# Performance work log

Hardware: AMD Instinct MI355X
Metric: run time of the kernel (lower is better)

The kernel has to match this reference:

```python
import jax, jax.numpy as jnp
import numpy as np
from jax import lax

H = 8          # num_heads
LAM = 4.0      # lambda_scale
POOL = 8       # pool_ratio (effective, N % POOL == 0)
NS_ITERS = 5
NS_EPS = 1e-4
WHITE_EPS = 1e-5


def _lap_kernel(x, y):
    # x: [B,H,n,D], y: [B,H,m,D] -> exp(-||x_i - y_j||_1 / LAM): [B,H,n,m]
    l1 = jnp.sum(jnp.abs(x[:, :, :, None, :] - y[:, :, None, :, :]), axis=-1)
    return jnp.exp(-l1 / LAM)


def setup_inputs() -> dict:
    key = jax.random.key(0)
    ks = jax.random.split(key, 8)
    B, N, C = 2, 1024, 512
    s = 0.05  # weight scale for realistic magnitudes
    return {
        "x": jax.random.normal(ks[0], (B, N, C), jnp.float32),
        "attention_mask": jnp.ones((B, N), jnp.float32),
        "qkv_w": jax.random.normal(ks[1], (3 * C, C), jnp.float32) * s,
        "qkv_b": jax.random.normal(ks[2], (3 * C,), jnp.float32) * s,
        "proj_w": jax.random.normal(ks[3], (C, C), jnp.float32) * s,
        "proj_b": jax.random.normal(ks[4], (C,), jnp.float32) * s,
        "dwc_w": jax.random.normal(ks[5], (C, 1, 3), jnp.float32) * s,
        "dwc_b": jax.random.normal(ks[6], (C,), jnp.float32) * s,
    }


def reference(x, attention_mask, qkv_w, qkv_b, proj_w, proj_b, dwc_w, dwc_b):
    B, N, C = x.shape
    D = C // H
    tm = attention_mask                      # [B,N]
    mh = tm[:, None, :, None]                # [B,1,N,1] broadcast over heads

    qkv = (x @ qkv_w.T + qkv_b).reshape(B, N, 3, H, D).transpose(2, 0, 3, 1, 4)
    q, k, v = qkv[0] * mh, qkv[1] * mh, qkv[2] * mh   # [B,H,N,D]

    # NOTE: faithful to source: raw reshape of [B,N,H*D] into [B,C,N]
    v_sp = v.transpose(0, 2, 1, 3).reshape(B, C, N)
    q_sp = q.transpose(0, 2, 1, 3).reshape(B, C, N)
    k_sp = k.transpose(0, 2, 1, 3).reshape(B, C, N)

    # depthwise conv1d, kernel 3, padding 1
    v_local = lax.conv_general_dilated(
        v_sp, dwc_w, window_strides=(1,), padding=[(1, 1)],
        feature_group_count=C, dimension_numbers=("NCH", "OIH", "NCH")
    ) + dwc_b[None, :, None]
    v_local = v_local.transpose(0, 2, 1) * tm[:, :, None]   # [B,N,C]

    p = POOL
    m = N // p
    pm = tm.reshape(B, 1, m, p).mean(-1)                    # [B,1,m]
    pms = jnp.clip(pm, 1e-6)
    q_pool = (q_sp * tm[:, None, :]).reshape(B, C, m, p).mean(-1) / pms
    k_pool = (k_sp * tm[:, None, :]).reshape(B, C, m, p).mean(-1) / pms
    lmask = (pm > 0).astype(x.dtype)[:, 0, :]               # [B,m]

    q_l = q_pool.transpose(0, 2, 1).reshape(B, m, H, D).transpose(0, 2, 1, 3)
    k_l = k_pool.transpose(0, 2, 1).reshape(B, m, H, D).transpose(0, 2, 1, 3)

    W = _lap_kernel(q_l, k_l)                               # [B,H,m,m]
    pair = lmask[:, None, :, None] * lmask[:, None, None, :]
    I = jnp.eye(m, dtype=x.dtype)[None, None]
    W = W * pair + I * (1.0 - pair)

    # Newton-Schulz pseudo-inverse
    W_eps = W + NS_EPS * I
    fro = jnp.sqrt(jnp.sum(W_eps * W_eps, axis=(-2, -1), keepdims=True))
    X = (2.0 / (fro + 1e-8)) * jnp.swapaxes(W_eps, -2, -1)
    for _ in range(NS_ITERS):
        X = X @ (2.0 * I - W_eps @ X)
    W_inv = X

    la_mask = lmask[:, None, None, :]                        # [B,1,1,m]
    C_q = _lap_kernel(q, k_l) * la_mask                      # [B,H,N,m]
    C_k = _lap_kernel(k, q_l) * la_mask                      # [B,H,N,m]

    # batch-statistics whitening of C_q over dims (0,2)
    qmask = tm[:, None, :, None]                             # [B,1,N,1]
    valid = jnp.clip(jnp.sum(qmask, axis=(0, 2), keepdims=True), 1.0)
    mu = jnp.sum(C_q * qmask, axis=(0, 2), keepdims=True) / valid
    cen = (C_q - mu) * qmask
    var = jnp.sum(cen * cen, axis=(0, 2), keepdims=True) / valid
    C_q_norm = ((C_q - mu) / jnp.sqrt(var + WHITE_EPS)) * qmask

    context = W_inv @ (jnp.swapaxes(C_k, -2, -1) @ v)        # [B,H,m,D]
    ga = (C_q_norm @ context) * mh                           # [B,H,N,D]
    ga = ga.transpose(0, 2, 1, 3).reshape(B, N, C)

    out = (ga + v_local) @ proj_w.T + proj_b
    return out * tm[:, :, None]
```

## Files before the change

### kernel.cpp

```cpp
#include <hip/hip_runtime.h>
#include <hip/hip_bf16.h>
#include <hip/hip_fp16.h>

#define Hh 8
#define Bz 2
#define Nn 1024
#define Cc 512
#define Dd 64
#define Mm 128
#define NS_EPS 1e-4f
#define WHITE_EPS 1e-5f
#define NEG_L2E_OVER_LAM (-0.3606737602222409f)

__device__ __forceinline__ float h2f(__half v) { return __half2float(v); }
__device__ __forceinline__ __half f2h(float v) { return __float2half(v); }
__device__ __forceinline__ float lapexp(float s) {
  return __builtin_amdgcn_exp2f(s * NEG_L2E_OVER_LAM);
}

typedef _Float16 half8 __attribute__((ext_vector_type(8)));
typedef _Float16 half4v __attribute__((ext_vector_type(4)));
typedef float float4v __attribute__((ext_vector_type(4)));

__global__ __launch_bounds__(256) void qkv_gemm(
    const float* __restrict__ x, const float* __restrict__ w,
    const float* __restrict__ bias, const float* __restrict__ tm,
    __half* __restrict__ Q, __half* __restrict__ K, __half* __restrict__ V) {
  __shared__ _Float16 As[128 * 40];
  __shared__ _Float16 Bs[128 * 40];
  int m0 = blockIdx.x * 128, n0 = blockIdx.y * 128;
  int tid = threadIdx.x;
  int lane = tid & 63, wv = tid >> 6;
  int wm = (wv >> 1) * 64, wn = (wv & 1) * 64;
  int l15 = lane & 15, quad = lane >> 4;
  int srow = tid >> 1, shalf = tid & 1;
  float4v acc[4][4] = {};
  for (int k0 = 0; k0 < 512; k0 += 32) {
    __syncthreads();
    {
      const float4* ga = (const float4*)(x + (size_t)(m0 + srow) * 512 + k0 + shalf * 16);
      const float4* gb = (const float4*)(w + (size_t)(n0 + srow) * 512 + k0 + shalf * 16);
      float4 a0 = ga[0], a1 = ga[1], a2 = ga[2], a3 = ga[3];
      float4 b0 = gb[0], b1 = gb[1], b2 = gb[2], b3 = gb[3];
      half8 ha0 = {(_Float16)a0.x, (_Float16)a0.y, (_Float16)a0.z, (_Float16)a0.w,
                   (_Float16)a1.x, (_Float16)a1.y, (_Float16)a1.z, (_Float16)a1.w};
      half8 ha1 = {(_Float16)a2.x, (_Float16)a2.y, (_Float16)a2.z, (_Float16)a2.w,
                   (_Float16)a3.x, (_Float16)a3.y, (_Float16)a3.z, (_Float16)a3.w};
      half8 hb0 = {(_Float16)b0.x, (_Float16)b0.y, (_Float16)b0.z, (_Float16)b0.w,
                   (_Float16)b1.x, (_Float16)b1.y, (_Float16)b1.z, (_Float16)b1.w};
      half8 hb1 = {(_Float16)b2.x, (_Float16)b2.y, (_Float16)b2.z, (_Float16)b2.w,
                   (_Float16)b3.x, (_Float16)b3.y, (_Float16)b3.z, (_Float16)b3.w};
      int lo = srow * 40 + shalf * 16;
      *(half8*)&As[lo] = ha0;
      *(half8*)&As[lo + 8] = ha1;
      *(half8*)&Bs[lo] = hb0;
      *(half8*)&Bs[lo + 8] = hb1;
    }
    __syncthreads();
    half8 a[4], b[4];
#pragma unroll
    for (int mt = 0; mt < 4; ++mt)
      a[mt] = *(const half8*)&As[(wm + mt * 16 + l15) * 40 + quad * 8];
#pragma unroll
    for (int nt = 0; nt < 4; ++nt)
      b[nt] = *(const half8*)&Bs[(wn + nt * 16 + l15) * 40 + quad * 8];
#pragma unroll
    for (int mt = 0; mt < 4; ++mt)
#pragma unroll
      for (int nt = 0; nt < 4; ++nt)
        acc[mt][nt] =
            __builtin_amdgcn_mfma_f32_16x16x32_f16(a[mt], b[nt], acc[mt][nt], 0, 0, 0);
  }
#pragma unroll
  for (int mt = 0; mt < 4; ++mt) {
#pragma unroll
    for (int r = 0; r < 4; ++r) {
      int row = m0 + wm + mt * 16 + quad * 4 + r;
      int b_ = row >> 10, n_ = row & 1023;
      float t = tm[b_ * 1024 + n_];
#pragma unroll
      for (int nt = 0; nt < 4; ++nt) {
        int c3 = n0 + wn + nt * 16 + l15;
        float v = (acc[mt][nt][r] + bias[c3]) * t;
        int sec = c3 >> 9, ch = c3 & 511;
        __half* dst = (sec == 0) ? Q : (sec == 1 ? K : V);
        dst[(size_t)b_ * (Nn * Cc) + (size_t)n_ * 512 + ch] = f2h(v);
      }
    }
  }
}

__global__ __launch_bounds__(256) void fused_phase1(
    const __half* __restrict__ Q, const __half* __restrict__ K,
    const __half* __restrict__ V, const float* __restrict__ tm,
    __half* __restrict__ Wh, float* __restrict__ KTVp,
    float* __restrict__ PS, __half* __restrict__ Pbuf) {
  __shared__ __align__(16) char smem[31232];
  int id = blockIdx.x;
  int tid = threadIdx.x;
  if (id < 512) {
    int jt = id & 3, bh = (id >> 2) & 15, nc = id >> 6;
    int b = bh >> 3, h = bh & 7;
    int j0 = jt * 32;
    float* kls = (float*)smem;
    float* Qs  = (float*)(smem + 8704);
    float* red = (float*)(smem + 17408);
    float* tms = (float*)(smem + 20480);
    float* pmi = (float*)(smem + 21504);
    float* lmv = (float*)(smem + 21632);
    int u0 = j0 * 8;
    tms[tid] = tm[b * 1024 + u0 + tid];
    __syncthreads();
    if (tid < 32) {
      float pm = 0.f;
#pragma unroll
      for (int i = 0; i < 8; ++i) pm += tms[tid * 8 + i];
      pm *= 0.125f;
      pmi[tid] = 0.125f / fmaxf(pm, 1e-6f);
      lmv[tid] = (pm > 0.f) ? 1.f : 0.f;
    }
    __syncthreads();
    {
      const __half* Kb = K + (size_t)b * (Nn * Cc) + (size_t)(h * 64) * 1024;
      int jl = tid >> 3, cq = tid & 7;
      float pv = pmi[jl];
      float r[8];
#pragma unroll
      for (int i = 0; i < 8; ++i) {
        int c = cq * 8 + i;
        half8 v = *(const half8*)(Kb + (size_t)c * 1024 + u0 + jl * 8);
        float s = 0.f;
#pragma unroll
        for (int xx = 0; xx < 8; ++xx) s += (float)v[xx] * tms[jl * 8 + xx];
        r[i] = s * pv;
      }
      float4 w0 = {r[0], r[1], r[2], r[3]};
      float4 w1 = {r[4], r[5], r[6], r[7]};
      *(float4*)&kls[jl * 68 + cq * 8] = w0;
      *(float4*)&kls[jl * 68 + cq * 8 + 4] = w1;
    }
    int sr = tid >> 3, sd8 = (tid & 7) * 8;
    int jq = tid & 15, nq = tid >> 4;
    float lmA = 0.f, lmB = 0.f;
    float aA1 = 0.f, aA2 = 0.f, aA3 = 0.f, aB1 = 0.f, aB2 = 0.f, aB3 = 0.f;
    int jA = j0 + jq * 2, jB = jA + 1;
    for (int nt = 0; nt < 4; ++nt) {
      int n0 = nc * 128 + nt * 32;
      __syncthreads();
      if (nt == 0) { lmA = lmv[jq * 2]; lmB = lmv[jq * 2 + 1]; }
      {
        size_t gi = (size_t)b * (Nn * Cc) + (size_t)(n0 + sr) * 512 + h * 64 + sd8;
        half8 kv = *(const half8*)(Q + gi);
        float4 k0 = {(float)kv[0], (float)kv[1], (float)kv[2], (float)kv[3]};
        float4 k1 = {(float)kv[4], (float)kv[5], (float)kv[6], (float)kv[7]};
        *(float4*)&Qs[sr * 68 + sd8] = k0;
        *(float4*)&Qs[sr * 68 + sd8 + 4] = k1;
      }
      __syncthreads();
      const float4* q0p = (const float4*)&kls[(jq * 2) * 68];
      const float4* q1p = (const float4*)&kls[(jq * 2 + 1) * 68];
      const float4* k0p = (const float4*)&Qs[(nq * 2) * 68];
      const float4* k1p = (const float4*)&Qs[(nq * 2 + 1) * 68];
      float s00 = 0.f, s01 = 0.f, s10 = 0.f, s11 = 0.f;
#pragma unroll
      for (int i = 0; i < 16; ++i) {
        int dq = (i + tid) & 15;
        float4 q0 = q0p[dq], q1 = q1p[dq];
        float4 k0 = k0p[dq], k1 = k1p[dq];
        s00 += fabsf(q0.x - k0.x) + fabsf(q0.y - k0.y) + fabsf(q0.z - k0.z) + fabsf(q0.w - k0.w);
        s01 += fabsf(q0.x - k1.x) + fabsf(q0.y - k1.y) + fabsf(q0.z - k1.z) + fabsf(q0.w - k1.w);
        s10 += fabsf(q1.x - k0.x) + fabsf(q1.y - k0.y) + fabsf(q1.z - k0.z) + fabsf(q1.w - k0.w);
        s11 += fabsf(q1.x - k1.x) + fabsf(q1.y - k1.y) + fabsf(q1.z - k1.z) + fabsf(q1.w - k1.w);
      }
      int nA = n0 + nq * 2, nB = nA + 1;
      float tA = tm[b * 1024 + nA], tB = tm[b * 1024 + nB];
      float xAa = lapexp(s00) * lmA;
      float xAb = lapexp(s01) * lmA;
      float xBa = lapexp(s10) * lmB;
      float xBb = lapexp(s11) * lmB;
      __half2 pA; pA.x = f2h(xAa); pA.y = f2h(xBa);
      __half2 pB; pB.x = f2h(xAb); pB.y = f2h(xBb);
      *(__half2*)&Pbuf[((size_t)bh * 1024 + nA) * 128 + jA] = pA;
      *(__half2*)&Pbuf[((size_t)bh * 1024 + nB) * 128 + jA] = pB;
      float xt;
      xt = xAa * tA; aA1 += xt; aA2 += xt * xt; aA3 += xt * tA;
      xt = xAb * tB; aA1 += xt; aA2 += xt * xt; aA3 += xt * tB;
      xt = xBa * tA; aB1 += xt; aB2 += xt * xt; aB3 += xt * tA;
      xt = xBb * tB; aB1 += xt; aB2 += xt * xt; aB3 += xt * tB;
    }
    int jl = jq * 2;
    red[(jl * 8 + nq) * 3 + 0] = aA1;
    red[(jl * 8 + nq) * 3 + 1] = aA2;
    red[(jl * 8 + nq) * 3 + 2] = aA3;
    red[((jl + 1) * 8 + nq) * 3 + 0] = aB1;
    red[((jl + 1) * 8 + nq) * 3 + 1] = aB2;
    red[((jl + 1) * 8 + nq) * 3 + 2] = aB3;
    __syncthreads();
    if (tid < 32) {
      float s1 = 0.f, s2 = 0.f, s3 = 0.f;
#pragma unroll
      for (int q = 0; q < 8; ++q) {
        s1 += red[(tid * 8 + q) * 3 + 0];
        s2 += red[(tid * 8 + q) * 3 + 1];
        s3 += red[(tid * 8 + q) * 3 + 2];
      }
      size_t base = ((size_t)(nc * 16 + bh) * 128 + j0 + tid) * 3;
      PS[base] = s1; PS[base + 1] = s2; PS[base + 2] = s3;
    }
  } else if (id < 1024) {
    int kid = id - 512;
    int jt = kid & 7, bh = (kid >> 3) & 15, nc = kid >> 7;
    int b = bh >> 3, h = bh & 7;
    int j0 = jt * 16;
    float* qls = (float*)smem;
    float* Ks  = (float*)(smem + 4352);
    float* Vs  = (float*)(smem + 13056);
    float* P   = (float*)(smem + 21760);
    float* tms = (float*)(smem + 24320);
    float* pmi = (float*)(smem + 24832);
    float* lmv = (float*)(smem + 24896);
    int u0 = j0 * 8;
    if (tid < 128) tms[tid] = tm[b * 1024 + u0 + tid];
    __syncthreads();
    if (tid < 16) {
      float pm = 0.f;
#pragma unroll
      for (int i = 0; i < 8; ++i) pm += tms[tid * 8 + i];
      pm *= 0.125f;
      pmi[tid] = 0.125f / fmaxf(pm, 1e-6f);
      lmv[tid] = (pm > 0.f) ? 1.f : 0.f;
    }
    __syncthreads();
    {
      const __half* Qb = Q + (size_t)b * (Nn * Cc) + (size_t)(h * 64) * 1024;
      int jl_ = tid >> 4, cq = tid & 15;
      float pv = pmi[jl_];
      float r[4];
#pragma unroll
      for (int i = 0; i < 4; ++i) {
        int c = cq * 4 + i;
        half8 v = *(const half8*)(Qb + (size_t)c * 1024 + u0 + jl_ * 8);
        float s = 0.f;
#pragma unroll
        for (int xx = 0; xx < 8; ++xx) s += (float)v[xx] * tms[jl_ * 8 + xx];
        r[i] = s * pv;
      }
      float4 w0 = {r[0], r[1], r[2], r[3]};
      *(float4*)&qls[jl_ * 68 + cq * 4] = w0;
    }
    int sr = tid >> 3, sd8 = (tid & 7) * 8;
    int jq = tid & 15, nq = tid >> 4;
    int jl = tid >> 4, dq4 = tid & 15;
    float acc[4] = {};
    for (int nt = 0; nt < 8; ++nt) {
      int n0 = nc * 256 + nt * 32;
      __syncthreads();
      {
        size_t gi = (size_t)b * (Nn * Cc) + (size_t)(n0 + sr) * 512 + h * 64 + sd8;
        half8 kv = *(const half8*)(K + gi);
        half8 vv = *(const half8*)(V + gi);
        float4 k0 = {(float)kv[0], (float)kv[1], (float)kv[2], (float)kv[3]};
        float4 k1 = {(float)kv[4], (float)kv[5], (float)kv[6], (float)kv[7]};
        float4 v0 = {(float)vv[0], (float)vv[1], (float)vv[2], (float)vv[3]};
        float4 v1 = {(float)vv[4], (float)vv[5], (float)vv[6], (float)vv[7]};
        *(float4*)&Ks[sr * 68 + sd8] = k0;
        *(float4*)&Ks[sr * 68 + sd8 + 4] = k1;
        *(float4*)&Vs[sr * 68 + sd8] = v0;
        *(float4*)&Vs[sr * 68 + sd8 + 4] = v1;
      }
      __syncthreads();
      {
        const float4* qp = (const float4*)&qls[jq * 68];
        const float4* k0p = (const float4*)&Ks[(nq * 2) * 68];
        const float4* k1p = (const float4*)&Ks[(nq * 2 + 1) * 68];
        float s0 = 0.f, s1 = 0.f;
#pragma unroll
        for (int i = 0; i < 16; ++i) {
          int dq = (i + tid) & 15;
          float4 qv = qp[dq];
          float4 k0 = k0p[dq], k1 = k1p[dq];
          s0 += fabsf(qv.x - k0.x) + fabsf(qv.y - k0.y) + fabsf(qv.z - k0.z) + fabsf(qv.w - k0.w);
          s1 += fabsf(qv.x - k1.x) + fabsf(qv.y - k1.y) + fabsf(qv.z - k1.z) + fabsf(qv.w - k1.w);
        }
        P[(nq * 2) * 20 + jq] = lapexp(s0);
        P[(nq * 2 + 1) * 20 + jq] = lapexp(s1);
      }
      __syncthreads();
      {
#pragma unroll 8
        for (int n = 0; n < 32; ++n) {
          float p = P[n * 20 + jl];
          float4 v = *(const float4*)&Vs[n * 68 + dq4 * 4];
          acc[0] += p * v.x; acc[1] += p * v.y; acc[2] += p * v.z; acc[3] += p * v.w;
        }
      }
    }
    {
      float lm = lmv[jl];
      float* dst = &KTVp[((size_t)nc * 16 + bh) * 8192 + (size_t)(j0 + jl) * 64 + dq4 * 4];
      float4 o = {acc[0] * lm, acc[1] * lm, acc[2] * lm, acc[3] * lm};
      *(float4*)dst = o;
    }
  } else {
    int wid = id - 1024;
    int it = wid >> 4, bh = wid & 15;
    int b = bh >> 3, h = bh & 7;
    int i0 = it * 16;
    _Float16* kls16 = (_Float16*)smem;
    float* qs  = (float*)(smem + 18432);
    float* pm2 = (float*)(smem + 22784);
    float* tms = (float*)(smem + 23808);
    _Float16* ps16 = (_Float16*)(smem + 23808);
    for (int e = tid; e < 1024; e += 256) tms[e] = tm[b * 1024 + e];
    __syncthreads();
    if (tid < 128) {
      float pm = 0.f;
#pragma unroll
      for (int i = 0; i < 8; ++i) pm += tms[tid * 8 + i];
      pm *= 0.125f;
      pm2[tid * 2] = 0.125f / fmaxf(pm, 1e-6f);
      pm2[tid * 2 + 1] = (pm > 0.f) ? 1.f : 0.f;
    }
    __syncthreads();
    {
      const __half* Kb = K + (size_t)b * (Nn * Cc) + (size_t)(h * 64) * 1024;
      const __half* Qb = Q + (size_t)b * (Nn * Cc) + (size_t)(h * 64) * 1024;
#pragma unroll
      for (int k = 0; k < 4; ++k) {
        int g = k * 256 + tid;
        int j = g >> 3, cq = g & 7;
        float pv = pm2[j * 2];
        _Float16 r[8];
#pragma unroll
        for (int i = 0; i < 8; ++i) {
          int c = cq * 8 + i;
          half8 v = *(const half8*)(Kb + (size_t)c * 1024 + j * 8);
          float s = 0.f;
#pragma unroll
          for (int xx = 0; xx < 8; ++xx) s += (float)v[xx] * tms[j * 8 + xx];
          r[i] = (_Float16)(s * pv);
        }
        half8 w0 = {r[0], r[1], r[2], r[3], r[4], r[5], r[6], r[7]};
        *(half8*)&kls16[j * 72 + cq * 8] = w0;
      }
      {
        int il = tid >> 4, cq = tid & 15;
        float pv = pm2[(i0 + il) * 2];
        float r[4];
#pragma unroll
        for (int i = 0; i < 4; ++i) {
          int c = cq * 4 + i;
          half8 v = *(const half8*)(Qb + (size_t)c * 1024 + (i0 + il) * 8);
          float s = 0.f;
#pragma unroll
          for (int xx = 0; xx < 8; ++xx) s += (float)v[xx] * tms[(i0 + il) * 8 + xx];
          r[i] = s * pv;
        }
        float4 w0 = {r[0], r[1], r[2], r[3]};
        *(float4*)&qs[il * 68 + cq * 4] = w0;
      }
    }
    __syncthreads();
    int jg = tid & 63, ng = tid >> 6;
    int j = jg * 2;
    const _Float16* kArow = &kls16[j * 72];
    const _Float16* kBrow = &kls16[(j + 1) * 72];
    float sA[4] = {}, sB[4] = {};
#pragma unroll
    for (int i = 0; i < 16; ++i) {
      int dq = (i + jg) & 15;
      half4v k4a = *(const half4v*)&kArow[dq * 4];
      half4v k4b = *(const half4v*)&kBrow[dq * 4];
      float4 ka = {(float)k4a[0], (float)k4a[1], (float)k4a[2], (float)k4a[3]};
      float4 kb = {(float)k4b[0], (float)k4b[1], (float)k4b[2], (float)k4b[3]};
#pragma unroll
      for (int r = 0; r < 4; ++r) {
        float4 qv = *(const float4*)&qs[(ng * 4 + r) * 68 + dq * 4];
        sA[r] += fabsf(qv.x - ka.x) + fabsf(qv.y - ka.y) + fabsf(qv.z - ka.z) + fabsf(qv.w - ka.w);
        sB[r] += fabsf(qv.x - kb.x) + fabsf(qv.y - kb.y) + fabsf(qv.z - kb.z) + fabsf(qv.w - kb.w);
      }
    }
    float lmA = pm2[j * 2 + 1], lmB = pm2[(j + 1) * 2 + 1];
#pragma unroll
    for (int r = 0; r < 4; ++r) {
      int i = i0 + ng * 4 + r;
      float lmi = pm2[i * 2 + 1];
      float prA = lmi * lmA, prB = lmi * lmB;
      float dA = (i == j) ? 1.f : 0.f;
      float dB = (i == j + 1) ? 1.f : 0.f;
      ps16[(ng * 4 + r) * 132 + j] =
          (_Float16)(lapexp(sA[r]) * prA + dA * (1.f - prA) + dA * NS_EPS);
      ps16[(ng * 4 + r) * 132 + j + 1] =
          (_Float16)(lapexp(sB[r]) * prB + dB * (1.f - prB) + dB * NS_EPS);
    }
    __syncthreads();
    for (int e = tid; e < 2048; e += 256) {
      _Float16 v = ps16[(e >> 7) * 132 + (e & 127)];
      Wh[(size_t)bh * (Mm * Mm) + (size_t)(i0 + (e >> 7)) * 128 + (e & 127)] =
          *(__half*)&v;
    }
  }
}

__global__ __launch_bounds__(1024) void fused_phase2(
    const __half* __restrict__ Wh, const float* __restrict__ KTVp,
    const float* __restrict__ PS, const float* __restrict__ tm,
    __half* __restrict__ CTX, float* __restrict__ MU, float* __restrict__ RS) {
  __shared__ __align__(16) char smem[143360];
  int tid = threadIdx.x;
  if (blockIdx.x < 16) {
    int bh = blockIdx.x;
    _Float16* Ws = (_Float16*)smem;
    _Float16* Xa = (_Float16*)(smem + 34816);
    _Float16* Xb = (_Float16*)(smem + 69632);
    _Float16* Tt = (_Float16*)(smem + 104448);
    float* red = (float*)(smem + 139264);
    const __half* Wb = Wh + (size_t)bh * 16384;
    float fro = 0.f;
    for (int e = tid; e < 16384; e += 1024) {
      float wv = h2f(Wb[e]);
      Ws[(e >> 7) * 136 + (e & 127)] = (_Float16)wv;
      fro += wv * wv;
    }
    red[tid] = fro;
    __syncthreads();
    for (int off = 512; off > 0; off >>= 1) {
      if (tid < off) red[tid] += red[tid + off];
      __syncthreads();
    }
    float scale = 2.f / (sqrtf(red[0]) + 1e-8f);
    for (int e = tid; e < 16384; e += 1024) {
      int i = e >> 7, k = e & 127;
      Xa[i * 136 + k] = (_Float16)(scale * (float)Ws[k * 136 + i]);
      Xb[i * 136 + k] = (_Float16)(scale * (float)Ws[i * 136 + k]);
    }
    __syncthreads();
    int lane = tid & 63, wv_ = tid >> 6;
    int wm = (wv_ >> 2) * 32, wn = (wv_ & 3) * 32;
    int l15 = lane & 15, quad = lane >> 4;
    for (int it = 0; it < 5; ++it) {
      {
        float4v acc[2][2] = {};
#pragma unroll
        for (int kt = 0; kt < 4; ++kt) {
          half8 a[2], b[2];
#pragma unroll
          for (int mt = 0; mt < 2; ++mt)
            a[mt] = *(const half8*)&Ws[(wm + mt * 16 + l15) * 136 + kt * 32 + quad * 8];
#pragma unroll
          for (int nt = 0; nt < 2; ++nt)
            b[nt] = *(const half8*)&Xb[(wn + nt * 16 + l15) * 136 + kt * 32 + quad * 8];
#pragma unroll
          for (int mt = 0; mt < 2; ++mt)
#pragma unroll
            for (int nt = 0; nt < 2; ++nt)
              acc[mt][nt] =
                  __builtin_amdgcn_mfma_f32_16x16x32_f16(a[mt], b[nt], acc[mt][nt], 0, 0, 0);
        }
#pragma unroll
        for (int mt = 0; mt < 2; ++mt)
#pragma unroll
          for (int r = 0; r < 4; ++r) {
            int i = wm + mt * 16 + quad * 4 + r;
#pragma unroll
            for (int nt = 0; nt < 2; ++nt) {
              int j = wn + nt * 16 + l15;
              Tt[j * 136 + i] = (_Float16)(((i == j) ? 2.f : 0.f) - acc[mt][nt][r]);
            }
          }
      }
      __syncthreads();
      {
        float4v acc[2][2] = {};
#pragma unroll
        for (int kt = 0; kt < 4; ++kt) {
          half8 a[2], b[2];
#pragma unroll
          for (int mt = 0; mt < 2; ++mt)
            a[mt] = *(const half8*)&Xa[(wm + mt * 16 + l15) * 136 + kt * 32 + quad * 8];
#pragma unroll
          for (int nt = 0; nt < 2; ++nt)
            b[nt] = *(const half8*)&Tt[(wn + nt * 16 + l15) * 136 + kt * 32 + quad * 8];
#pragma unroll
          for (int mt = 0; mt < 2; ++mt)
#pragma unroll
            for (int nt = 0; nt < 2; ++nt)
              acc[mt][nt] =
                  __builtin_amdgcn_mfma_f32_16x16x32_f16(a[mt], b[nt], acc[mt][nt], 0, 0, 0);
        }
        __syncthreads();
#pragma unroll
        for (int mt = 0; mt < 2; ++mt)
#pragma unroll
          for (int r = 0; r < 4; ++r) {
            int i = wm + mt * 16 + quad * 4 + r;
#pragma unroll
            for (int nt = 0; nt < 2; ++nt) {
              int j = wn + nt * 16 + l15;
              _Float16 v = (_Float16)acc[mt][nt][r];
              Xa[i * 136 + j] = v;
              Xb[j * 136 + i] = v;
            }
          }
      }
      __syncthreads();
    }
    float* KTVs = (float*)smem;
    for (int e = tid; e < 8192; e += 1024) {
      float s = KTVp[(size_t)bh * 8192 + e];
#pragma unroll
      for (int nc = 1; nc < 4; ++nc) s += KTVp[((size_t)nc * 16 + bh) * 8192 + e];
      KTVs[(e >> 6) * 68 + (e & 63)] = s;
    }
    __syncthreads();
    int i = tid >> 3, d0 = (tid & 7) * 8;
    float a0 = 0.f, a1 = 0.f, a2 = 0.f, a3 = 0.f;
    float a4 = 0.f, a5 = 0.f, a6 = 0.f, a7 = 0.f;
#pragma unroll 4
    for (int j = 0; j < 128; ++j) {
      float xv = (float)Xa[i * 136 + j];
      float4 k0 = *(const float4*)&KTVs[j * 68 + d0];
      float4 k1 = *(const float4*)&KTVs[j * 68 + d0 + 4];
      a0 += xv * k0.x; a1 += xv * k0.y; a2 += xv * k0.z; a3 += xv * k0.w;
      a4 += xv * k1.x; a5 += xv * k1.y; a6 += xv * k1.z; a7 += xv * k1.w;
    }
    half8 hout = {(_Float16)a0, (_Float16)a1, (_Float16)a2, (_Float16)a3,
                  (_Float16)a4, (_Float16)a5, (_Float16)a6, (_Float16)a7};
    *(half8*)(CTX + (size_t)bh * 8192 + (size_t)i * 64 + d0) = hout;
  } else {
    float (*red2)[2] = (float(*)[2])smem;
    float* ts = (float*)(smem + 8192);
    float a = 0.f, c = 0.f;
    for (int i = tid; i < 2048; i += 1024) { float t = tm[i]; a += t; c += t * t; }
    red2[tid][0] = a; red2[tid][1] = c;
    __syncthreads();
    for (int off = 512; off > 0; off >>= 1) {
      if (tid < off) { red2[tid][0] += red2[tid + off][0]; red2[tid][1] += red2[tid + off][1]; }
      __syncthreads();
    }
    if (tid == 0) { ts[0] = red2[0][0]; ts[1] = red2[0][1]; }
    __syncthreads();
    int hj = tid;
    int h = hj >> 7, j = hj & 127;
    float s1 = 0.f, s2 = 0.f, s3 = 0.f;
#pragma unroll
    for (int nc = 0; nc < 8; ++nc)
#pragma unroll
      for (int b = 0; b < 2; ++b) {
        const float* p = PS + ((size_t)(nc * 16 + b * 8 + h) * 128 + j) * 3;
        s1 += p[0]; s2 += p[1]; s3 += p[2];
      }
    float valid = fmaxf(ts[0], 1.f);
    float mu = s1 / valid;
    float var = (s2 - 2.f * mu * s3 + mu * mu * ts[1]) / valid;
    var = fmaxf(var, 0.f);
    MU[hj] = mu;
    RS[hj] = rsqrtf(var + WHITE_EPS);
  }
}

__global__ __launch_bounds__(256) void ga_fused(
    const __half* __restrict__ Pbuf, const float* __restrict__ MU,
    const float* __restrict__ RS, const __half* __restrict__ CTXg,
    const __half* __restrict__ V, const float* __restrict__ dwc_w,
    const float* __restrict__ dwc_b, const float* __restrict__ tm,
    __half* __restrict__ VL) {
  int bh = blockIdx.y;
  int b = bh >> 3, h = bh & 7;
  int n0 = blockIdx.x * 32;
  __shared__ __half Ps[32][130];
  __shared__ __align__(16) __half2 ctx2[128][32];
  __shared__ float musr[128][2];
  int tid = threadIdx.x;
  for (int e = tid; e < 4096; e += 256)
    Ps[e >> 7][e & 127] = Pbuf[((size_t)bh * 1024 + n0 + (e >> 7)) * 128 + (e & 127)];
  {
    const __half2* cg = (const __half2*)(CTXg + (size_t)bh * 8192);
    for (int e = tid; e < 4096; e += 256) ctx2[e >> 5][e & 31] = cg[e];
  }
  if (tid < 128) { musr[tid][0] = MU[h * 128 + tid]; musr[tid][1] = RS[h * 128 + tid]; }
  __syncthreads();
  int nn = tid >> 4, dq = tid & 15;
  float acc[2][4] = {};
#pragma unroll 2
  for (int j = 0; j < 128; ++j) {
    float mu = musr[j][0], rs = musr[j][1];
    uint2 cc = *(const uint2*)&ctx2[j][dq * 2];
    __half2 c01 = __builtin_bit_cast(__half2, cc.x);
    __half2 c23 = __builtin_bit_cast(__half2, cc.y);
    float c0 = h2f(c01.x), c1 = h2f(c01.y), c2 = h2f(c23.x), c3 = h2f(c23.y);
#pragma unroll
    for (int rr = 0; rr < 2; ++rr) {
      float pj = (h2f(Ps[nn + rr * 16][j]) - mu) * rs;
      acc[rr][0] += pj * c0; acc[rr][1] += pj * c1;
      acc[rr][2] += pj * c2; acc[rr][3] += pj * c3;
    }
  }
#pragma unroll
  for (int rr = 0; rr < 2; ++rr) {
    int t = n0 + nn + rr * 16;
    float tmv = tm[b * 1024 + t];
    float t2 = tmv * tmv;
    float o[4] = {acc[rr][0] * t2, acc[rr][1] * t2, acc[rr][2] * t2, acc[rr][3] * t2};
#pragma unroll
    for (int q = 0; q < 4; ++q) {
      int c = h * 64 + dq * 4 + q;
      float vacc = dwc_b[c];
#pragma unroll
      for (int k = 0; k < 3; ++k) {
        int u = t - 1 + k;
        if (u >= 0 && u < 1024) {
          int n = 2 * c + (u >> 9), ch = u & 511;
          vacc += dwc_w[c * 3 + k] * h2f(V[(size_t)b * (Nn * Cc) + (size_t)n * 512 + ch]);
        }
      }
      o[q] += vacc * tmv;
    }
    size_t base = (size_t)b * (Nn * Cc) + (size_t)t * 512 + h * 64 + dq * 4;
    VL[base] = f2h(o[0]);
    VL[base + 1] = f2h(o[1]);
    VL[base + 2] = f2h(o[2]);
    VL[base + 3] = f2h(o[3]);
  }
}

__global__ __launch_bounds__(256) void proj_gemm(
    const __half* __restrict__ Ain, const float* __restrict__ w,
    const float* __restrict__ bias, const float* __restrict__ tm,
    float* __restrict__ out) {
  __shared__ _Float16 As[64 * 40];
  __shared__ _Float16 Bs[64 * 40];
  int m0 = blockIdx.x * 64, n0 = blockIdx.y * 64;
  int tid = threadIdx.x;
  int lane = tid & 63, wv = tid >> 6;
  int wm = (wv >> 1) * 32, wn = (wv & 1) * 32;
  int l15 = lane & 15, quad = lane >> 4;
  int srow = tid >> 2, scol = (tid & 3) * 8;
  float4v acc[2][2] = {};
  for (int k0 = 0; k0 < 512; k0 += 32) {
    __syncthreads();
    {
      half8 ha = *(const half8*)(Ain + (size_t)(m0 + srow) * 512 + k0 + scol);
      const float4* gb = (const float4*)(w + (size_t)(n0 + srow) * 512 + k0 + scol);
      float4 b0 = gb[0], b1 = gb[1];
      half8 hb = {(_Float16)b0.x, (_Float16)b0.y, (_Float16)b0.z, (_Float16)b0.w,
                  (_Float16)b1.x, (_Float16)b1.y, (_Float16)b1.z, (_Float16)b1.w};
      int lo = srow * 40 + scol;
      *(half8*)&As[lo] = ha;
      *(half8*)&Bs[lo] = hb;
    }
    __syncthreads();
    half8 a[2], b[2];
#pragma unroll
    for (int mt = 0; mt < 2; ++mt)
      a[mt] = *(const half8*)&As[(wm + mt * 16 + l15) * 40 + quad * 8];
#pragma unroll
    for (int nt = 0; nt < 2; ++nt)
      b[nt] = *(const half8*)&Bs[(wn + nt * 16 + l15) * 40 + quad * 8];
#pragma unroll
    for (int mt = 0; mt < 2; ++mt)
#pragma unroll
      for (int nt = 0; nt < 2; ++nt)
        acc[mt][nt] =
            __builtin_amdgcn_mfma_f32_16x16x32_f16(a[mt], b[nt], acc[mt][nt], 0, 0, 0);
  }
#pragma unroll
  for (int mt = 0; mt < 2; ++mt) {
#pragma unroll
    for (int r = 0; r < 4; ++r) {
      int row = m0 + wm + mt * 16 + quad * 4 + r;
      int b_ = row >> 10, n_ = row & 1023;
      float t = tm[b_ * 1024 + n_];
#pragma unroll
      for (int nt = 0; nt < 2; ++nt) {
        int co = n0 + wn + nt * 16 + l15;
        out[(size_t)row * 512 + co] = (acc[mt][nt][r] + bias[co]) * t;
      }
    }
  }
}

extern "C" void kernel_launch(void* const* d_in, const int* in_sizes, int n_in,
                              void* d_out, int out_size, void* d_ws, size_t ws_size,
                              hipStream_t stream) {
  const float* x      = (const float*)d_in[0];
  const float* tm     = (const float*)d_in[1];
  const float* qkv_w  = (const float*)d_in[2];
  const float* qkv_b  = (const float*)d_in[3];
  const float* proj_w = (const float*)d_in[4];
  const float* proj_b = (const float*)d_in[5];
  const float* dwc_w  = (const float*)d_in[6];
  const float* dwc_b  = (const float*)d_in[7];
  float* out = (float*)d_out;

  char* wsb = (char*)d_ws;
  __half* Qh  = (__half*)(wsb + 0);
  __half* Kh  = (__half*)(wsb + 2097152);
  __half* Vh  = (__half*)(wsb + 4194304);
  __half* VLh = (__half*)(wsb + 6291456);
  float*  KTVp = (float*)(wsb + 6291456);
  float*  MU  = (float*)(wsb + 8913920);
  float*  RS  = (float*)(wsb + 8918016);
  __half* CTX = (__half*)(wsb + 8922112);
  float*  PS  = (float*)(wsb + 9184256);
  __half* Wh  = (__half*)(wsb + 9380864);

  __half* Pbuf = (__half*)d_out;

  qkv_gemm<<<dim3(16, 12), 256, 0, stream>>>(x, qkv_w, qkv_b, tm, Qh, Kh, Vh);
  fused_phase1<<<1152, 256, 0, stream>>>(Qh, Kh, Vh, tm, Wh, KTVp, PS, Pbuf);
  fused_phase2<<<17, 1024, 0, stream>>>(Wh, KTVp, PS, tm, CTX, MU, RS);
  ga_fused<<<dim3(32, 16), 256, 0, stream>>>(Pbuf, MU, RS, CTX, Vh, dwc_w, dwc_b, tm, VLh);
  proj_gemm<<<dim3(32, 8), 256, 0, stream>>>(VLh, proj_w, proj_b, tm, out);
}
```

Before: 197.5 us.

## Compute L1 distances in packed fp16 with dot2 and reorder block roles

Replaces the fp32 L1-distance inner loops in all three phase-1 block roles with packed fp16 subtraction, a sign-bit mask and fdot2 accumulation into fp32. Operands are now staged in LDS as fp16 instead of being widened to fp32, which cuts shared-memory footprint and traffic and the count of ALU instructions per distance. The W-matrix blocks, previously last in the grid, are moved to the front so the heavier per-block work starts early. The cost is extra rounding in the differences, since pooled q/k values are rounded to fp16 before subtraction, which could change accuracy in the exponent.

```diff
diff --git a/kernel.cpp b/kernel.cpp
--- a/kernel.cpp
+++ b/kernel.cpp
@@ -20,7 +20,22 @@
 
 typedef _Float16 half8 __attribute__((ext_vector_type(8)));
 typedef _Float16 half4v __attribute__((ext_vector_type(4)));
+typedef _Float16 half2v __attribute__((ext_vector_type(2)));
+typedef unsigned int uint4v __attribute__((ext_vector_type(4)));
 typedef float float4v __attribute__((ext_vector_type(4)));
+
+__device__ __forceinline__ float l1dot(half8 a, half8 b, float s) {
+  half8 d = a - b;
+  uint4v u = __builtin_bit_cast(uint4v, d);
+  u &= 0x7FFF7FFFu;
+  const half2v one = {(_Float16)1.f, (_Float16)1.f};
+#pragma unroll
+  for (int p = 0; p < 4; ++p) {
+    half2v dv = __builtin_bit_cast(half2v, (unsigned int)u[p]);
+    s = __builtin_amdgcn_fdot2(dv, one, s, false);
+  }
+  return s;
+}
 
 __global__ __launch_bounds__(256) void qkv_gemm(
     const float* __restrict__ x, const float* __restrict__ w,
@@ -95,19 +110,115 @@
     const __half* __restrict__ V, const float* __restrict__ tm,
     __half* __restrict__ Wh, float* __restrict__ KTVp,
     float* __restrict__ PS, __half* __restrict__ Pbuf) {
-  __shared__ __align__(16) char smem[31232];
+  __shared__ __align__(16) char smem[25984];
   int id = blockIdx.x;
   int tid = threadIdx.x;
-  if (id < 512) {
-    int jt = id & 3, bh = (id >> 2) & 15, nc = id >> 6;
+  if (id < 128) {
+    int it = id >> 4, bh = id & 15;
+    int b = bh >> 3, h = bh & 7;
+    int i0 = it * 16;
+    _Float16* kls16 = (_Float16*)smem;
+    _Float16* qs16 = (_Float16*)(smem + 18432);
+    float* pm2 = (float*)(smem + 20736);
+    float* tms = (float*)(smem + 21760);
+    _Float16* ps16 = (_Float16*)(smem + 21760);
+    for (int e = tid; e < 1024; e += 256) tms[e] = tm[b * 1024 + e];
+    __syncthreads();
+    if (tid < 128) {
+      float pm = 0.f;
+#pragma unroll
+      for (int i = 0; i < 8; ++i) pm += tms[tid * 8 + i];
+      pm *= 0.125f;
+      pm2[tid * 2] = 0.125f / fmaxf(pm, 1e-6f);
+      pm2[tid * 2 + 1] = (pm > 0.f) ? 1.f : 0.f;
+    }
+    __syncthreads();
+    {
+      const __half* Kb = K + (size_t)b * (Nn * Cc) + (size_t)(h * 64) * 1024;
+      const __half* Qb = Q + (size_t)b * (Nn * Cc) + (size_t)(h * 64) * 1024;
+#pragma unroll
+      for (int k = 0; k < 4; ++k) {
+        int g = k * 256 + tid;
+        int j = g >> 3, cq = g & 7;
+        float pv = pm2[j * 2];
+        _Float16 r[8];
+#pragma unroll
+        for (int i = 0; i < 8; ++i) {
+          int c = cq * 8 + i;
+          half8 v = *(const half8*)(Kb + (size_t)c * 1024 + j * 8);
+          float s = 0.f;
+#pragma unroll
+          for (int xx = 0; xx < 8; ++xx) s += (float)v[xx] * tms[j * 8 + xx];
+          r[i] = (_Float16)(s * pv);
+        }
+        half8 w0 = {r[0], r[1], r[2], r[3], r[4], r[5], r[6], r[7]};
+        *(half8*)&kls16[j * 72 + cq * 8] = w0;
+      }
+      {
+        int il = tid >> 4, cq = tid & 15;
+        float pv = pm2[(i0 + il) * 2];
+        _Float16 r[4];
+#pragma unroll
+        for (int i = 0; i < 4; ++i) {
+          int c = cq * 4 + i;
+          half8 v = *(const half8*)(Qb + (size_t)c * 1024 + (i0 + il) * 8);
+          float s = 0.f;
+#pragma unroll
+          for (int xx = 0; xx < 8; ++xx) s += (float)v[xx] * tms[(i0 + il) * 8 + xx];
+          r[i] = (_Float16)(s * pv);
+        }
+        half4v w0 = {r[0], r[1], r[2], r[3]};
+        *(half4v*)&qs16[il * 72 + cq * 4] = w0;
+      }
+    }
+    __syncthreads();
+    int jg = tid & 63, ng = tid >> 6;
+    int j = jg * 2;
+    const half8* kAp = (const half8*)&kls16[j * 72];
+    const half8* kBp = (const half8*)&kls16[(j + 1) * 72];
+    float sA[4] = {}, sB[4] = {};
+#pragma unroll
+    for (int i = 0; i < 8; ++i) {
+      int dq = (i + jg) & 7;
+      half8 ka = kAp[dq];
+      half8 kb = kBp[dq];
+#pragma unroll
+      for (int r = 0; r < 4; ++r) {
+        half8 qv = *(const half8*)&qs16[(ng * 4 + r) * 72 + dq * 8];
+        sA[r] = l1dot(qv, ka, sA[r]);
+        sB[r] = l1dot(qv, kb, sB[r]);
+      }
+    }
+    float lmA = pm2[j * 2 + 1], lmB = pm2[(j + 1) * 2 + 1];
+#pragma unroll
+    for (int r = 0; r < 4; ++r) {
+      int i = i0 + ng * 4 + r;
+      float lmi = pm2[i * 2 + 1];
+      float prA = lmi * lmA, prB = lmi * lmB;
+      float dA = (i == j) ? 1.f : 0.f;
+      float dB = (i == j + 1) ? 1.f : 0.f;
+      ps16[(ng * 4 + r) * 132 + j] =
+          (_Float16)(lapexp(sA[r]) * prA + dA * (1.f - prA) + dA * NS_EPS);
+      ps16[(ng * 4 + r) * 132 + j + 1] =
+          (_Float16)(lapexp(sB[r]) * prB + dB * (1.f - prB) + dB * NS_EPS);
+    }
+    __syncthreads();
+    for (int e = tid; e < 2048; e += 256) {
+      _Float16 v = ps16[(e >> 7) * 132 + (e & 127)];
+      Wh[(size_t)bh * (Mm * Mm) + (size_t)(i0 + (e >> 7)) * 128 + (e & 127)] =
+          *(__half*)&v;
+    }
+  } else if (id < 640) {
+    int sid = id - 128;
+    int jt = sid & 3, bh = (sid >> 2) & 15, nc = sid >> 6;
     int b = bh >> 3, h = bh & 7;
     int j0 = jt * 32;
-    float* kls = (float*)smem;
-    float* Qs  = (float*)(smem + 8704);
-    float* red = (float*)(smem + 17408);
-    float* tms = (float*)(smem + 20480);
-    float* pmi = (float*)(smem + 21504);
-    float* lmv = (float*)(smem + 21632);
+    _Float16* kls16 = (_Float16*)smem;
+    _Float16* Qs16 = (_Float16*)(smem + 4608);
+    float* red = (float*)(smem + 9216);
+    float* tms = (float*)(smem + 12288);
+    float* pmi = (float*)(smem + 13312);
+    float* lmv = (float*)(smem + 13440);
     int u0 = j0 * 8;
     tms[tid] = tm[b * 1024 + u0 + tid];
     __syncthreads();
@@ -124,7 +235,7 @@
       const __half* Kb = K + (size_t)b * (Nn * Cc) + (size_t)(h * 64) * 1024;
       int jl = tid >> 3, cq = tid & 7;
       float pv = pmi[jl];
-      float r[8];
+      _Float16 r[8];
 #pragma unroll
       for (int i = 0; i < 8; ++i) {
         int c = cq * 8 + i;
@@ -132,12 +243,10 @@
         float s = 0.f;
 #pragma unroll
         for (int xx = 0; xx < 8; ++xx) s += (float)v[xx] * tms[jl * 8 + xx];
-        r[i] = s * pv;
-      }
-      float4 w0 = {r[0], r[1], r[2], r[3]};
-      float4 w1 = {r[4], r[5], r[6], r[7]};
-      *(float4*)&kls[jl * 68 + cq * 8] = w0;
-      *(float4*)&kls[jl * 68 + cq * 8 + 4] = w1;
+        r[i] = (_Float16)(s * pv);
+      }
+      half8 w0 = {r[0], r[1], r[2], r[3], r[4], r[5], r[6], r[7]};
+      *(half8*)&kls16[jl * 72 + cq * 8] = w0;
     }
     int sr = tid >> 3, sd8 = (tid & 7) * 8;
     int jq = tid & 15, nq = tid >> 4;
@@ -151,26 +260,23 @@
       {
         size_t gi = (size_t)b * (Nn * Cc) + (size_t)(n0 + sr) * 512 + h * 64 + sd8;
         half8 kv = *(const half8*)(Q + gi);
-        float4 k0 = {(float)kv[0], (float)kv[1], (float)kv[2], (float)kv[3]};
-        float4 k1 = {(float)kv[4], (float)kv[5], (float)kv[6], (float)kv[7]};
-        *(float4*)&Qs[sr * 68 + sd8] = k0;
-        *(float4*)&Qs[sr * 68 + sd8 + 4] = k1;
-      }
-      __syncthreads();
-      const float4* q0p = (const float4*)&kls[(jq * 2) * 68];
-      const float4* q1p = (const float4*)&kls[(jq * 2 + 1) * 68];
-      const float4* k0p = (const float4*)&Qs[(nq * 2) * 68];
-      const float4* k1p = (const float4*)&Qs[(nq * 2 + 1) * 68];
+        *(half8*)&Qs16[sr * 72 + sd8] = kv;
+      }
+      __syncthreads();
+      const half8* q0p = (const half8*)&kls16[(jq * 2) * 72];
+      const half8* q1p = (const half8*)&kls16[(jq * 2 + 1) * 72];
+      const half8* k0p = (const half8*)&Qs16[(nq * 2) * 72];
+      const half8* k1p = (const half8*)&Qs16[(nq * 2 + 1) * 72];
       float s00 = 0.f, s01 = 0.f, s10 = 0.f, s11 = 0.f;
 #pragma unroll
-      for (int i = 0; i < 16; ++i) {
-        int dq = (i + tid) & 15;
-        float4 q0 = q0p[dq], q1 = q1p[dq];
-        float4 k0 = k0p[dq], k1 = k1p[dq];
-        s00 += fabsf(q0.x - k0.x) + fabsf(q0.y - k0.y) + fabsf(q0.z - k0.z) + fabsf(q0.w - k0.w);
-        s01 += fabsf(q0.x - k1.x) + fabsf(q0.y - k1.y) + fabsf(q0.z - k1.z) + fabsf(q0.w - k1.w);
-        s10 += fabsf(q1.x - k0.x) + fabsf(q1.y - k0.y) + fabsf(q1.z - k0.z) + fabsf(q1.w - k0.w);
-        s11 += fabsf(q1.x - k1.x) + fabsf(q1.y - k1.y) + fabsf(q1.z - k1.z) + fabsf(q1.w - k1.w);
+      for (int i = 0; i < 8; ++i) {
+        int dq = (i + tid) & 7;
+        half8 q0 = q0p[dq], q1 = q1p[dq];
+        half8 k0 = k0p[dq], k1 = k1p[dq];
+        s00 = l1dot(q0, k0, s00);
+        s01 = l1dot(q0, k1, s01);
+        s10 = l1dot(q1, k0, s10);
+        s11 = l1dot(q1, k1, s11);
       }
       int nA = n0 + nq * 2, nB = nA + 1;
       float tA = tm[b * 1024 + nA], tB = tm[b * 1024 + nB];
@@ -207,18 +313,18 @@
       size_t base = ((size_t)(nc * 16 + bh) * 128 + j0 + tid) * 3;
       PS[base] = s1; PS[base + 1] = s2; PS[base + 2] = s3;
     }
-  } else if (id < 1024) {
-    int kid = id - 512;
+  } else {
+    int kid = id - 640;
     int jt = kid & 7, bh = (kid >> 3) & 15, nc = kid >> 7;
     int b = bh >> 3, h = bh & 7;
     int j0 = jt * 16;
-    float* qls = (float*)smem;
-    float* Ks  = (float*)(smem + 4352);
-    float* Vs  = (float*)(smem + 13056);
-    float* P   = (float*)(smem + 21760);
-    float* tms = (float*)(smem + 24320);
-    float* pmi = (float*)(smem + 24832);
-    float* lmv = (float*)(smem + 24896);
+    _Float16* qls16 = (_Float16*)smem;
+    _Float16* Ks16 = (_Float16*)(smem + 2304);
+    float* Vs = (float*)(smem + 6912);
+    float* P = (float*)(smem + 15616);
+    float* tms = (float*)(smem + 18176);
+    float* pmi = (float*)(smem + 18688);
+    float* lmv = (float*)(smem + 18752);
     int u0 = j0 * 8;
     if (tid < 128) tms[tid] = tm[b * 1024 + u0 + tid];
     __syncthreads();
@@ -235,7 +341,7 @@
       const __half* Qb = Q + (size_t)b * (Nn * Cc) + (size_t)(h * 64) * 1024;
       int jl_ = tid >> 4, cq = tid & 15;
       float pv = pmi[jl_];
-      float r[4];
+      _Float16 r[4];
 #pragma unroll
       for (int i = 0; i < 4; ++i) {
         int c = cq * 4 + i;
@@ -243,10 +349,10 @@
         float s = 0.f;
 #pragma unroll
         for (int xx = 0; xx < 8; ++xx) s += (float)v[xx] * tms[jl_ * 8 + xx];
-        r[i] = s * pv;
-      }
-      float4 w0 = {r[0], r[1], r[2], r[3]};
-      *(float4*)&qls[jl_ * 68 + cq * 4] = w0;
+        r[i] = (_Float16)(s * pv);
+      }
+      half4v w0 = {r[0], r[1], r[2], r[3]};
+      *(half4v*)&qls16[jl_ * 72 + cq * 4] = w0;
     }
     int sr = tid >> 3, sd8 = (tid & 7) * 8;
     int jq = tid & 15, nq = tid >> 4;
@@ -259,28 +365,25 @@
         size_t gi = (size_t)b * (Nn * Cc) + (size_t)(n0 + sr) * 512 + h * 64 + sd8;
         half8 kv = *(const half8*)(K + gi);
         half8 vv = *(const half8*)(V + gi);
-        float4 k0 = {(float)kv[0], (float)kv[1], (float)kv[2], (float)kv[3]};
-        float4 k1 = {(float)kv[4], (float)kv[5], (float)kv[6], (float)kv[7]};
+        *(half8*)&Ks16[sr * 72 + sd8] = kv;
         float4 v0 = {(float)vv[0], (float)vv[1], (float)vv[2], (float)vv[3]};
         float4 v1 = {(float)vv[4], (float)vv[5], (float)vv[6], (float)vv[7]};
-        *(float4*)&Ks[sr * 68 + sd8] = k0;
-        *(float4*)&Ks[sr * 68 + sd8 + 4] = k1;
         *(float4*)&Vs[sr * 68 + sd8] = v0;
         *(float4*)&Vs[sr * 68 + sd8 + 4] = v1;
       }
       __syncthreads();
       {
-        const float4* qp = (const float4*)&qls[jq * 68];
-        const float4* k0p = (const float4*)&Ks[(nq * 2) * 68];
-        const float4* k1p = (const float4*)&Ks[(nq * 2 + 1) * 68];
+        const half8* qp = (const half8*)&qls16[jq * 72];
+        const half8* k0p = (const half8*)&Ks16[(nq * 2) * 72];
+        const half8* k1p = (const half8*)&Ks16[(nq * 2 + 1) * 72];
         float s0 = 0.f, s1 = 0.f;
 #pragma unroll
-        for (int i = 0; i < 16; ++i) {
-          int dq = (i + tid) & 15;
-          float4 qv = qp[dq];
-          float4 k0 = k0p[dq], k1 = k1p[dq];
-          s0 += fabsf(qv.x - k0.x) + fabsf(qv.y - k0.y) + fabsf(qv.z - k0.z) + fabsf(qv.w - k0.w);
-          s1 += fabsf(qv.x - k1.x) + fabsf(qv.y - k1.y) + fabsf(qv.z - k1.z) + fabsf(qv.w - k1.w);
+        for (int i = 0; i < 8; ++i) {
+          int dq = (i + tid) & 7;
+          half8 qv = qp[dq];
+          half8 k0 = k0p[dq], k1 = k1p[dq];
+          s0 = l1dot(qv, k0, s0);
+          s1 = l1dot(qv, k1, s1);
         }
         P[(nq * 2) * 20 + jq] = lapexp(s0);
         P[(nq * 2 + 1) * 20 + jq] = lapexp(s1);
@@ -300,104 +403,6 @@
       float* dst = &KTVp[((size_t)nc * 16 + bh) * 8192 + (size_t)(j0 + jl) * 64 + dq4 * 4];
       float4 o = {acc[0] * lm, acc[1] * lm, acc[2] * lm, acc[3] * lm};
       *(float4*)dst = o;
-    }
-  } else {
-    int wid = id - 1024;
-    int it = wid >> 4, bh = wid & 15;
-    int b = bh >> 3, h = bh & 7;
-    int i0 = it * 16;
-    _Float16* kls16 = (_Float16*)smem;
-    float* qs  = (float*)(smem + 18432);
-    float* pm2 = (float*)(smem + 22784);
-    float* tms = (float*)(smem + 23808);
-    _Float16* ps16 = (_Float16*)(smem + 23808);
-    for (int e = tid; e < 1024; e += 256) tms[e] = tm[b * 1024 + e];
-    __syncthreads();
-    if (tid < 128) {
-      float pm = 0.f;
-#pragma unroll
-      for (int i = 0; i < 8; ++i) pm += tms[tid * 8 + i];
-      pm *= 0.125f;
-      pm2[tid * 2] = 0.125f / fmaxf(pm, 1e-6f);
-      pm2[tid * 2 + 1] = (pm > 0.f) ? 1.f : 0.f;
-    }
-    __syncthreads();
-    {
-      const __half* Kb = K + (size_t)b * (Nn * Cc) + (size_t)(h * 64) * 1024;
-      const __half* Qb = Q + (size_t)b * (Nn * Cc) + (size_t)(h * 64) * 1024;
-#pragma unroll
-      for (int k = 0; k < 4; ++k) {
-        int g = k * 256 + tid;
-        int j = g >> 3, cq = g & 7;
-        float pv = pm2[j * 2];
-        _Float16 r[8];
-#pragma unroll
-        for (int i = 0; i < 8; ++i) {
-          int c = cq * 8 + i;
-          half8 v = *(const half8*)(Kb + (size_t)c * 1024 + j * 8);
-          float s = 0.f;
-#pragma unroll
-          for (int xx = 0; xx < 8; ++xx) s += (float)v[xx] * tms[j * 8 + xx];
-          r[i] = (_Float16)(s * pv);
-        }
-        half8 w0 = {r[0], r[1], r[2], r[3], r[4], r[5], r[6], r[7]};
-        *(half8*)&kls16[j * 72 + cq * 8] = w0;
-      }
-      {
-        int il = tid >> 4, cq = tid & 15;
-        float pv = pm2[(i0 + il) * 2];
-        float r[4];
-#pragma unroll
-        for (int i = 0; i < 4; ++i) {
-          int c = cq * 4 + i;
-          half8 v = *(const half8*)(Qb + (size_t)c * 1024 + (i0 + il) * 8);
-          float s = 0.f;
-#pragma unroll
-          for (int xx = 0; xx < 8; ++xx) s += (float)v[xx] * tms[(i0 + il) * 8 + xx];
-          r[i] = s * pv;
-        }
-        float4 w0 = {r[0], r[1], r[2], r[3]};
-        *(float4*)&qs[il * 68 + cq * 4] = w0;
-      }
-    }
-    __syncthreads();
-    int jg = tid & 63, ng = tid >> 6;
-    int j = jg * 2;
-    const _Float16* kArow = &kls16[j * 72];
-    const _Float16* kBrow = &kls16[(j + 1) * 72];
-    float sA[4] = {}, sB[4] = {};
-#pragma unroll
-    for (int i = 0; i < 16; ++i) {
-      int dq = (i + jg) & 15;
-      half4v k4a = *(const half4v*)&kArow[dq * 4];
-      half4v k4b = *(const half4v*)&kBrow[dq * 4];
-      float4 ka = {(float)k4a[0], (float)k4a[1], (float)k4a[2], (float)k4a[3]};
-      float4 kb = {(float)k4b[0], (float)k4b[1], (float)k4b[2], (float)k4b[3]};
-#pragma unroll
-      for (int r = 0; r < 4; ++r) {
-        float4 qv = *(const float4*)&qs[(ng * 4 + r) * 68 + dq * 4];
-        sA[r] += fabsf(qv.x - ka.x) + fabsf(qv.y - ka.y) + fabsf(qv.z - ka.z) + fabsf(qv.w - ka.w);
-        sB[r] += fabsf(qv.x - kb.x) + fabsf(qv.y - kb.y) + fabsf(qv.z - kb.z) + fabsf(qv.w - kb.w);
-      }
-    }
-    float lmA = pm2[j * 2 + 1], lmB = pm2[(j + 1) * 2 + 1];
-#pragma unroll
-    for (int r = 0; r < 4; ++r) {
-      int i = i0 + ng * 4 + r;
-      float lmi = pm2[i * 2 + 1];
-      float prA = lmi * lmA, prB = lmi * lmB;
-      float dA = (i == j) ? 1.f : 0.f;
-      float dB = (i == j + 1) ? 1.f : 0.f;
-      ps16[(ng * 4 + r) * 132 + j] =
-          (_Float16)(lapexp(sA[r]) * prA + dA * (1.f - prA) + dA * NS_EPS);
-      ps16[(ng * 4 + r) * 132 + j + 1] =
-          (_Float16)(lapexp(sB[r]) * prB + dB * (1.f - prB) + dB * NS_EPS);
-    }
-    __syncthreads();
-    for (int e = tid; e < 2048; e += 256) {
-      _Float16 v = ps16[(e >> 7) * 132 + (e & 127)];
-      Wh[(size_t)bh * (Mm * Mm) + (size_t)(i0 + (e >> 7)) * 128 + (e & 127)] =
-          *(__half*)&v;
     }
   }
 }
```

Result: slower. 201.7 us (+2.2%).
